# Performance work log

Measured on AMD Instinct MI355X. Metric: run time of the kernel, lower is better.

The kernel has to match this reference:

```python
import jax, jax.numpy as jnp
import numpy as np

ELT_BATCH = 64            # number of candidate elements (rows)
OBS_PER_ELT = 100_000     # observations per element (uniform row_lengths)
DATA_SIZE = ELT_BATCH * OBS_PER_ELT
THRESH_DEG = 2.0
THRESH_HIT_PROB_POST = 0.95


def _deg2dist(deg):
    # chord length on unit sphere subtended by angle `deg`
    return 2.0 * np.sin(np.radians(deg) / 2.0)


def setup_inputs() -> dict:
    key = jax.random.key(0)
    k1, k2, k3, k4 = jax.random.split(key, 4)
    # observed unit directions
    u_obs = jax.random.normal(k1, (DATA_SIZE, 3), dtype=jnp.float32)
    u_obs = u_obs / jnp.linalg.norm(u_obs, axis=-1, keepdims=True)
    # predicted directions = observed + small perturbation so a realistic
    # fraction of observations fall inside the 2-degree threshold
    noise = 0.01 * jax.random.normal(k2, (DATA_SIZE, 3), dtype=jnp.float32)
    u_pred = u_obs + noise
    u_pred = u_pred / jnp.linalg.norm(u_pred, axis=-1, keepdims=True)
    # mixture-model params per element: hit fraction h in (0.1, 0.9), decay lam in (1, 10)
    h = 0.1 + 0.8 * jax.random.uniform(k3, (ELT_BATCH,), dtype=jnp.float32)
    lam = 1.0 + 9.0 * jax.random.uniform(k4, (ELT_BATCH,), dtype=jnp.float32)
    # squared chord-distance threshold per element (constant buffer in the layer)
    thresh_s2 = jnp.full((ELT_BATCH,), np.float32(_deg2dist(THRESH_DEG) ** 2), dtype=jnp.float32)
    return {"u_pred": u_pred, "u_obs": u_obs, "h": h, "lam": lam, "thresh_s2": thresh_s2}


def reference(u_pred, u_obs, h, lam, thresh_s2):
    B = thresh_s2.shape[0]
    n_per = u_pred.shape[0] // B  # uniform row_lengths
    seg_ids = jnp.repeat(jnp.arange(B, dtype=jnp.int32), n_per)  # [data_size]

    # squared chord distance per observation
    du = u_pred - u_obs                                # [N, 3]
    s2 = jnp.sum(jnp.square(du), axis=-1)              # [N]

    thresh_rep = jnp.repeat(thresh_s2, n_per)          # [N]
    h_rep = jnp.repeat(h, n_per)                       # [N]
    lam_rep = jnp.repeat(lam, n_per)                   # [N]

    is_close = s2 < thresh_rep                         # [N] bool
    v = s2 / thresh_rep                                # normalized squared distance in [0,1) where close

    # truncated-exponential mixture model
    emlx = jnp.exp(-lam_rep * v)
    p_hit_cond = emlx * lam_rep / (1.0 - jnp.exp(-lam_rep))
    p_hit = h_rep * p_hit_cond
    p = p_hit + (1.0 - h_rep)

    # mask instead of boolean_mask: excluded entries contribute 0 to segment sums
    log_p = jnp.where(is_close, jnp.log(p), 0.0)
    p_hit_post = p_hit / p
    is_real_hit = p_hit_post > THRESH_HIT_PROB_POST
    p_hit_filtered = jnp.where(is_close & is_real_hit, p_hit_post, 0.0)

    log_like = jax.ops.segment_sum(log_p, seg_ids, num_segments=B)        # [B]
    hits = jax.ops.segment_sum(p_hit_filtered, seg_ids, num_segments=B)   # [B]
    hits_raw = hits  # original code sums p_hit_filtered for both outputs
    return (log_like, hits, hits_raw)
```

## Files before the change

kernel.cpp:

```cpp
#include <hip/hip_runtime.h>


constexpr int ELT_BATCH       = 64;
constexpr int OBS_PER_ELT     = 100000;
constexpr int F4_PER_SEG      = OBS_PER_ELT * 3 / 4;
constexpr int CHUNK_F4        = 63;
constexpr int CHUNKS_PER_SEG  = (F4_PER_SEG + CHUNK_F4 - 1) / CHUNK_F4;
constexpr int BLOCKS_PER_SEG  = 32;
constexpr int BLOCK           = 256;
constexpr int WAVES_PER_BLOCK = BLOCK / 64;
constexpr int WAVES_PER_SEG   = BLOCKS_PER_SEG * WAVES_PER_BLOCK;
constexpr int UNROLL          = 4;

__device__ __forceinline__ float wave_reduce_sum(float v) {
    #pragma unroll
    for (int off = 32; off > 0; off >>= 1)
        v += __shfl_down(v, off, 64);
    return v;
}

__global__ __launch_bounds__(BLOCK, 8) void TrajectoryScore_58145267253396_kernel(
    const float4* __restrict__ pred4,
    const float4* __restrict__ obs4,
    const float*  __restrict__ h_arr,
    const float*  __restrict__ lam_arr,
    const float*  __restrict__ th_arr,
    float*        __restrict__ out)
{
    const int seg        = blockIdx.x / BLOCKS_PER_SEG;
    const int blk_in_seg = blockIdx.x % BLOCKS_PER_SEG;
    const int tid  = threadIdx.x;
    const int lane = tid & 63;
    const int wave = tid >> 6;
    const int wseg = blk_in_seg * WAVES_PER_BLOCK + wave;

    const float h      = h_arr[seg];
    const float lam    = lam_arr[seg];
    const float th     = th_arr[seg];
    const float inv_th = 1.0f / th;
    const float coef   = h * lam / (1.0f - __expf(-lam));
    const float omh    = 1.0f - h;
    const float nli    = -lam * inv_th;

    const int  m  = lane % 3;
    const bool m0 = (m == 0);
    const bool m1 = (m == 1);

    const int seg_f4 = seg * F4_PER_SEG;

    float ll = 0.0f;
    float hs = 0.0f;

    for (int c0 = wseg; c0 < CHUNKS_PER_SEG; c0 += UNROLL * WAVES_PER_SEG) {
        float4 A[UNROLL], B[UNROLL];
        int    act[UNROLL];

        #pragma unroll
        for (int u = 0; u < UNROLL; ++u) {
            const int c = c0 + u * WAVES_PER_SEG;
            if (c < CHUNKS_PER_SEG) {
                const int base = c * CHUNK_F4;
                const int idx  = seg_f4 + min(base + lane, F4_PER_SEG - 1);
                A[u]   = pred4[idx];
                B[u]   = obs4[idx];
                act[u] = min(CHUNK_F4, F4_PER_SEG - base);
            } else {
                act[u] = 0;
            }
        }

        #pragma unroll
        for (int u = 0; u < UNROLL; ++u) {
            if (act[u] != 0) {
                const float4 a = A[u], b = B[u];
                const float d0 = a.x - b.x, d1 = a.y - b.y, d2 = a.z - b.z, d3 = a.w - b.w;
                const float q0 = d0 * d0, q1 = d1 * d1, q2 = d2 * d2, q3 = d3 * d3;

                const float head = m1 ? (q0 + q1) : q0;
                const float hn   = __shfl_down(head, 1, 64);

                const float t12 = q1 + q2;
                const float s2A = m0 ? (q0 + t12) : (m1 ? (q2 + q3 + hn) : (t12 + q3));
                const float s2B = q3 + hn;

                const bool lv = lane < act[u];
                {
                    const float e  = __expf(nli * s2A);
                    const float ph = coef * e;
                    const float p  = ph + omh;
                    const float lp = __logf(p);
                    const float po = ph / p;
                    const bool  cl = (s2A < th) && lv;
                    ll += cl ? lp : 0.0f;
                    hs += (cl && po > 0.95f) ? po : 0.0f;
                }
                {
                    const float e  = __expf(nli * s2B);
                    const float ph = coef * e;
                    const float p  = ph + omh;
                    const float lp = __logf(p);
                    const float po = ph / p;
                    const bool  cl = (s2B < th) && lv && m0;
                    ll += cl ? lp : 0.0f;
                    hs += (cl && po > 0.95f) ? po : 0.0f;
                }
            }
        }
    }

    ll = wave_reduce_sum(ll);
    hs = wave_reduce_sum(hs);

    __shared__ float sll[WAVES_PER_BLOCK];
    __shared__ float shs[WAVES_PER_BLOCK];
    if (lane == 0) { sll[wave] = ll; shs[wave] = hs; }
    __syncthreads();
    if (tid == 0) {
        float L = 0.0f, H = 0.0f;
        #pragma unroll
        for (int w = 0; w < WAVES_PER_BLOCK; ++w) { L += sll[w]; H += shs[w]; }
        atomicAdd(&out[seg], L);
        atomicAdd(&out[ELT_BATCH + seg], H);
        atomicAdd(&out[2 * ELT_BATCH + seg], H);
    }
}

extern "C" void kernel_launch(void* const* d_in, const int* in_sizes, int n_in,
                              void* d_out, int out_size, void* d_ws, size_t ws_size,
                              hipStream_t stream) {
    const float4* pred4   = (const float4*)d_in[0];
    const float4* obs4    = (const float4*)d_in[1];
    const float*  h_arr   = (const float*)d_in[2];
    const float*  lam_arr = (const float*)d_in[3];
    const float*  th_arr  = (const float*)d_in[4];
    float* out = (float*)d_out;

    hipMemsetAsync(out, 0, out_size * sizeof(float), stream);

    dim3 grid(ELT_BATCH * BLOCKS_PER_SEG);
    dim3 block(BLOCK);
    TrajectoryScore_58145267253396_kernel<<<grid, block, 0, stream>>>(
        pred4, obs4, h_arr, lam_arr, th_arr, out);
}
```

Measured before the change: 179.4 us.

## Software-pipeline chunk loads with double-buffered prefetch over a fixed unrolled loop

Replaces the strided unrolled loop with a fixed five-iteration, fully unrolled loop. It prefetches the next pair of chunks into a second set of registers before evaluating the current pair, and a sched_barrier keeps the loads issued ahead of the math. Chunks past the segment end are masked by a non-positive active count and clamped load indices. The aim is to hide global-load latency behind the exp/log work, at the cost of more registers and a few redundant clamped loads in the last iteration.

Measured after the change: 179.1 us. About the same (-0.2%).

```diff
diff --git a/kernel.cpp b/kernel.cpp
--- a/kernel.cpp
+++ b/kernel.cpp
@@ -10,13 +10,53 @@
 constexpr int BLOCK           = 256;
 constexpr int WAVES_PER_BLOCK = BLOCK / 64;
 constexpr int WAVES_PER_SEG   = BLOCKS_PER_SEG * WAVES_PER_BLOCK;
-constexpr int UNROLL          = 4;
+constexpr int PAIR_STRIDE     = 2 * WAVES_PER_SEG;
+constexpr int ITERS           = 5;
 
 __device__ __forceinline__ float wave_reduce_sum(float v) {
     #pragma unroll
     for (int off = 32; off > 0; off >>= 1)
         v += __shfl_down(v, off, 64);
     return v;
+}
+
+__device__ __forceinline__ void eval_chunk(
+    const float4 a, const float4 b, const int act,
+    const int lane, const bool m0, const bool m1,
+    const float nli, const float coef, const float omh, const float th,
+    float& ll, float& hs)
+{
+    const float d0 = a.x - b.x, d1 = a.y - b.y, d2 = a.z - b.z, d3 = a.w - b.w;
+    const float q0 = d0 * d0, q1 = d1 * d1, q2 = d2 * d2, q3 = d3 * d3;
+
+    const float head = m1 ? (q0 + q1) : q0;
+    const float hn   = __shfl_down(head, 1, 64);
+
+    const float t12 = q1 + q2;
+    const float s2A = m0 ? (q0 + t12) : (m1 ? (q2 + q3 + hn) : (t12 + q3));
+    const float s2B = q3 + hn;
+
+    const bool lv = lane < act;
+    {
+        const float e  = __expf(nli * s2A);
+        const float ph = coef * e;
+        const float p  = ph + omh;
+        const float lp = __logf(p);
+        const float po = ph / p;
+        const bool  cl = (s2A < th) && lv;
+        ll += cl ? lp : 0.0f;
+        hs += (cl && po > 0.95f) ? po : 0.0f;
+    }
+    {
+        const float e  = __expf(nli * s2B);
+        const float ph = coef * e;
+        const float p  = ph + omh;
+        const float lp = __logf(p);
+        const float po = ph / p;
+        const bool  cl = (s2B < th) && lv && m0;
+        ll += cl ? lp : 0.0f;
+        hs += (cl && po > 0.95f) ? po : 0.0f;
+    }
 }
 
 __global__ __launch_bounds__(BLOCK, 8) void TrajectoryScore_58145267253396_kernel(
@@ -51,61 +91,31 @@
     float ll = 0.0f;
     float hs = 0.0f;
 
-    for (int c0 = wseg; c0 < CHUNKS_PER_SEG; c0 += UNROLL * WAVES_PER_SEG) {
-        float4 A[UNROLL], B[UNROLL];
-        int    act[UNROLL];
+    auto ld = [&](int c, float4& A, float4& B) {
+        const int idx = seg_f4 + min(c * CHUNK_F4 + lane, F4_PER_SEG - 1);
+        A = pred4[idx];
+        B = obs4[idx];
+    };
 
-        #pragma unroll
-        for (int u = 0; u < UNROLL; ++u) {
-            const int c = c0 + u * WAVES_PER_SEG;
-            if (c < CHUNKS_PER_SEG) {
-                const int base = c * CHUNK_F4;
-                const int idx  = seg_f4 + min(base + lane, F4_PER_SEG - 1);
-                A[u]   = pred4[idx];
-                B[u]   = obs4[idx];
-                act[u] = min(CHUNK_F4, F4_PER_SEG - base);
-            } else {
-                act[u] = 0;
-            }
-        }
+    float4 A0, B0, A1, B1, A0n, B0n, A1n, B1n;
+    ld(wseg,                   A0, B0);
+    ld(wseg + WAVES_PER_SEG,   A1, B1);
 
-        #pragma unroll
-        for (int u = 0; u < UNROLL; ++u) {
-            if (act[u] != 0) {
-                const float4 a = A[u], b = B[u];
-                const float d0 = a.x - b.x, d1 = a.y - b.y, d2 = a.z - b.z, d3 = a.w - b.w;
-                const float q0 = d0 * d0, q1 = d1 * d1, q2 = d2 * d2, q3 = d3 * d3;
+    #pragma unroll
+    for (int it = 0; it < ITERS; ++it) {
+        const int cn = wseg + (it + 1) * PAIR_STRIDE;
+        ld(cn,                 A0n, B0n);
+        ld(cn + WAVES_PER_SEG, A1n, B1n);
+        __builtin_amdgcn_sched_barrier(0);
 
-                const float head = m1 ? (q0 + q1) : q0;
-                const float hn   = __shfl_down(head, 1, 64);
+        const int c = wseg + it * PAIR_STRIDE;
+        eval_chunk(A0, B0, F4_PER_SEG - c * CHUNK_F4 < CHUNK_F4 ? F4_PER_SEG - c * CHUNK_F4 : CHUNK_F4,
+                   lane, m0, m1, nli, coef, omh, th, ll, hs);
+        eval_chunk(A1, B1, F4_PER_SEG - (c + WAVES_PER_SEG) * CHUNK_F4 < CHUNK_F4
+                              ? F4_PER_SEG - (c + WAVES_PER_SEG) * CHUNK_F4 : CHUNK_F4,
+                   lane, m0, m1, nli, coef, omh, th, ll, hs);
 
-                const float t12 = q1 + q2;
-                const float s2A = m0 ? (q0 + t12) : (m1 ? (q2 + q3 + hn) : (t12 + q3));
-                const float s2B = q3 + hn;
-
-                const bool lv = lane < act[u];
-                {
-                    const float e  = __expf(nli * s2A);
-                    const float ph = coef * e;
-                    const float p  = ph + omh;
-                    const float lp = __logf(p);
-                    const float po = ph / p;
-                    const bool  cl = (s2A < th) && lv;
-                    ll += cl ? lp : 0.0f;
-                    hs += (cl && po > 0.95f) ? po : 0.0f;
-                }
-                {
-                    const float e  = __expf(nli * s2B);
-                    const float ph = coef * e;
-                    const float p  = ph + omh;
-                    const float lp = __logf(p);
-                    const float po = ph / p;
-                    const bool  cl = (s2B < th) && lv && m0;
-                    ll += cl ? lp : 0.0f;
-                    hs += (cl && po > 0.95f) ? po : 0.0f;
-                }
-            }
-        }
+        A0 = A0n; B0 = B0n; A1 = A1n; B1 = B1n;
     }
 
     ll = wave_reduce_sum(ll);
```

## Split into flat s2 computation pass and per-segment evaluation pass via workspace

Applied to the files above, without the earlier changes.

Splits the single fused kernel in two. The first kernel walks the whole flattened float4 stream, computes each observation's squared chord distance and writes it to a workspace buffer. The second kernel reads that buffer per segment and evaluates the mixture model and reductions. The intent is to decouple the streaming loads from the transcendental math and drop per-segment chunk-boundary handling, at the cost of an extra 25.6 MB write and read through the workspace plus a second launch.

Measured after the change: 190.5 us. +6.2%, slower.

```diff
diff --git a/kernel.cpp b/kernel.cpp
--- a/kernel.cpp
+++ b/kernel.cpp
@@ -1,16 +1,17 @@
 #include <hip/hip_runtime.h>
 
 
-constexpr int ELT_BATCH       = 64;
-constexpr int OBS_PER_ELT     = 100000;
-constexpr int F4_PER_SEG      = OBS_PER_ELT * 3 / 4;
-constexpr int CHUNK_F4        = 63;
-constexpr int CHUNKS_PER_SEG  = (F4_PER_SEG + CHUNK_F4 - 1) / CHUNK_F4;
-constexpr int BLOCKS_PER_SEG  = 32;
-constexpr int BLOCK           = 256;
-constexpr int WAVES_PER_BLOCK = BLOCK / 64;
-constexpr int WAVES_PER_SEG   = BLOCKS_PER_SEG * WAVES_PER_BLOCK;
-constexpr int UNROLL          = 4;
+constexpr int ELT_BATCH   = 64;
+constexpr int OBS_PER_ELT = 100000;
+constexpr int N_F4_TOTAL  = ELT_BATCH * OBS_PER_ELT * 3 / 4;
+constexpr int CHUNK_F4    = 63;
+constexpr int CHUNK_OBS   = 84;
+constexpr int N_CHUNKS    = (N_F4_TOTAL + CHUNK_F4 - 1) / CHUNK_F4;
+constexpr int BLOCK       = 256;
+constexpr int P1_BLOCKS   = 1024;
+constexpr int P1_WAVES    = P1_BLOCKS * (BLOCK / 64);
+constexpr int P2_BLOCKS_PER_SEG = 8;
+constexpr int S2_F4_PER_SEG     = OBS_PER_ELT / 4;
 
 __device__ __forceinline__ float wave_reduce_sum(float v) {
     #pragma unroll
@@ -19,20 +20,73 @@
     return v;
 }
 
-__global__ __launch_bounds__(BLOCK, 8) void TrajectoryScore_58145267253396_kernel(
+__device__ __forceinline__ void s2_chunk(
+    const float4 a, const float4 b, const int c,
+    const int lane, const int g, const bool m0, const bool m1,
+    float* __restrict__ s2out)
+{
+    const float d0 = a.x - b.x, d1 = a.y - b.y, d2 = a.z - b.z, d3 = a.w - b.w;
+    const float q0 = d0 * d0, q1 = d1 * d1, q2 = d2 * d2, q3 = d3 * d3;
+
+    const float head = m1 ? (q0 + q1) : q0;
+    const float hn   = __shfl_down(head, 1, 64);
+
+    const float t12 = q1 + q2;
+    const float s2A = m0 ? (q0 + t12) : (m1 ? (q2 + q3 + hn) : (t12 + q3));
+    const float s2B = q3 + hn;
+
+    const int act  = min(CHUNK_F4, N_F4_TOTAL - c * CHUNK_F4);
+    const int base = c * CHUNK_OBS;
+    const int offA = 4 * g + (m0 ? 0 : (m1 ? 2 : 3));
+
+    if (lane < act)         s2out[base + offA]      = s2A;
+    if (m0 && lane < act)   s2out[base + 4 * g + 1] = s2B;
+}
+
+__global__ __launch_bounds__(BLOCK) void TrajectoryScore_58145267253396_kernel(
     const float4* __restrict__ pred4,
     const float4* __restrict__ obs4,
-    const float*  __restrict__ h_arr,
-    const float*  __restrict__ lam_arr,
-    const float*  __restrict__ th_arr,
-    float*        __restrict__ out)
+    float*        __restrict__ s2out)
 {
-    const int seg        = blockIdx.x / BLOCKS_PER_SEG;
-    const int blk_in_seg = blockIdx.x % BLOCKS_PER_SEG;
-    const int tid  = threadIdx.x;
+    const int tid   = threadIdx.x;
+    const int lane  = tid & 63;
+    const int gwave = blockIdx.x * (BLOCK / 64) + (tid >> 6);
+
+    const int  m  = lane % 3;
+    const bool m0 = (m == 0);
+    const bool m1 = (m == 1);
+    const int  g  = lane / 3;
+
+    auto addr = [&](int c) { return min(c * CHUNK_F4 + lane, N_F4_TOTAL - 1); };
+
+    int c = gwave;
+    for (; c + P1_WAVES < N_CHUNKS; c += 2 * P1_WAVES) {
+        const int c1 = c + P1_WAVES;
+        const int i0 = addr(c), i1 = addr(c1);
+        const float4 a0 = pred4[i0], b0 = obs4[i0];
+        const float4 a1 = pred4[i1], b1 = obs4[i1];
+        s2_chunk(a0, b0, c,  lane, g, m0, m1, s2out);
+        s2_chunk(a1, b1, c1, lane, g, m0, m1, s2out);
+    }
+    for (; c < N_CHUNKS; c += P1_WAVES) {
+        const int i0 = addr(c);
+        const float4 a0 = pred4[i0], b0 = obs4[i0];
+        s2_chunk(a0, b0, c, lane, g, m0, m1, s2out);
+    }
+}
+
+__global__ __launch_bounds__(BLOCK) void TrajectoryScore_58145267253396_eval_kernel(
+    const float* __restrict__ s2buf,
+    const float* __restrict__ h_arr,
+    const float* __restrict__ lam_arr,
+    const float* __restrict__ th_arr,
+    float*       __restrict__ out)
+{
+    const int seg = blockIdx.x / P2_BLOCKS_PER_SEG;
+    const int blk = blockIdx.x % P2_BLOCKS_PER_SEG;
+    const int tid = threadIdx.x;
     const int lane = tid & 63;
     const int wave = tid >> 6;
-    const int wseg = blk_in_seg * WAVES_PER_BLOCK + wave;
 
     const float h      = h_arr[seg];
     const float lam    = lam_arr[seg];
@@ -42,83 +96,38 @@
     const float omh    = 1.0f - h;
     const float nli    = -lam * inv_th;
 
-    const int  m  = lane % 3;
-    const bool m0 = (m == 0);
-    const bool m1 = (m == 1);
-
-    const int seg_f4 = seg * F4_PER_SEG;
+    const float4* s2_4 = reinterpret_cast<const float4*>(s2buf) + seg * S2_F4_PER_SEG;
 
     float ll = 0.0f;
     float hs = 0.0f;
 
-    for (int c0 = wseg; c0 < CHUNKS_PER_SEG; c0 += UNROLL * WAVES_PER_SEG) {
-        float4 A[UNROLL], B[UNROLL];
-        int    act[UNROLL];
+    auto eval1 = [&](float s2) {
+        const float e  = __expf(nli * s2);
+        const float ph = coef * e;
+        const float p  = ph + omh;
+        const float lp = __logf(p);
+        const float po = ph / p;
+        const bool  cl = (s2 < th);
+        ll += cl ? lp : 0.0f;
+        hs += (cl && po > 0.95f) ? po : 0.0f;
+    };
 
-        #pragma unroll
-        for (int u = 0; u < UNROLL; ++u) {
-            const int c = c0 + u * WAVES_PER_SEG;
-            if (c < CHUNKS_PER_SEG) {
-                const int base = c * CHUNK_F4;
-                const int idx  = seg_f4 + min(base + lane, F4_PER_SEG - 1);
-                A[u]   = pred4[idx];
-                B[u]   = obs4[idx];
-                act[u] = min(CHUNK_F4, F4_PER_SEG - base);
-            } else {
-                act[u] = 0;
-            }
-        }
-
-        #pragma unroll
-        for (int u = 0; u < UNROLL; ++u) {
-            if (act[u] != 0) {
-                const float4 a = A[u], b = B[u];
-                const float d0 = a.x - b.x, d1 = a.y - b.y, d2 = a.z - b.z, d3 = a.w - b.w;
-                const float q0 = d0 * d0, q1 = d1 * d1, q2 = d2 * d2, q3 = d3 * d3;
-
-                const float head = m1 ? (q0 + q1) : q0;
-                const float hn   = __shfl_down(head, 1, 64);
-
-                const float t12 = q1 + q2;
-                const float s2A = m0 ? (q0 + t12) : (m1 ? (q2 + q3 + hn) : (t12 + q3));
-                const float s2B = q3 + hn;
-
-                const bool lv = lane < act[u];
-                {
-                    const float e  = __expf(nli * s2A);
-                    const float ph = coef * e;
-                    const float p  = ph + omh;
-                    const float lp = __logf(p);
-                    const float po = ph / p;
-                    const bool  cl = (s2A < th) && lv;
-                    ll += cl ? lp : 0.0f;
-                    hs += (cl && po > 0.95f) ? po : 0.0f;
-                }
-                {
-                    const float e  = __expf(nli * s2B);
-                    const float ph = coef * e;
-                    const float p  = ph + omh;
-                    const float lp = __logf(p);
-                    const float po = ph / p;
-                    const bool  cl = (s2B < th) && lv && m0;
-                    ll += cl ? lp : 0.0f;
-                    hs += (cl && po > 0.95f) ? po : 0.0f;
-                }
-            }
-        }
+    for (int i = blk * BLOCK + tid; i < S2_F4_PER_SEG; i += P2_BLOCKS_PER_SEG * BLOCK) {
+        const float4 s = s2_4[i];
+        eval1(s.x); eval1(s.y); eval1(s.z); eval1(s.w);
     }
 
     ll = wave_reduce_sum(ll);
     hs = wave_reduce_sum(hs);
 
-    __shared__ float sll[WAVES_PER_BLOCK];
-    __shared__ float shs[WAVES_PER_BLOCK];
+    __shared__ float sll[BLOCK / 64];
+    __shared__ float shs[BLOCK / 64];
     if (lane == 0) { sll[wave] = ll; shs[wave] = hs; }
     __syncthreads();
     if (tid == 0) {
         float L = 0.0f, H = 0.0f;
         #pragma unroll
-        for (int w = 0; w < WAVES_PER_BLOCK; ++w) { L += sll[w]; H += shs[w]; }
+        for (int w = 0; w < BLOCK / 64; ++w) { L += sll[w]; H += shs[w]; }
         atomicAdd(&out[seg], L);
         atomicAdd(&out[ELT_BATCH + seg], H);
         atomicAdd(&out[2 * ELT_BATCH + seg], H);
@@ -133,12 +142,15 @@
     const float*  h_arr   = (const float*)d_in[2];
     const float*  lam_arr = (const float*)d_in[3];
     const float*  th_arr  = (const float*)d_in[4];
-    float* out = (float*)d_out;
+    float* out  = (float*)d_out;
+    float* s2ws = (float*)d_ws;
 
     hipMemsetAsync(out, 0, out_size * sizeof(float), stream);
 
-    dim3 grid(ELT_BATCH * BLOCKS_PER_SEG);
-    dim3 block(BLOCK);
-    TrajectoryScore_58145267253396_kernel<<<grid, block, 0, stream>>>(
-        pred4, obs4, h_arr, lam_arr, th_arr, out);
+    TrajectoryScore_58145267253396_kernel<<<dim3(P1_BLOCKS), dim3(BLOCK), 0, stream>>>(
+        pred4, obs4, s2ws);
+
+    TrajectoryScore_58145267253396_eval_kernel<<<dim3(ELT_BATCH * P2_BLOCKS_PER_SEG),
+                                                 dim3(BLOCK), 0, stream>>>(
+        s2ws, h_arr, lam_arr, th_arr, out);
 }
```
